# Performance work log

Hardware: AMD Instinct MI355X
Metric: run time of the kernel (lower is better)

The kernel has to match this reference:

```python
import jax, jax.numpy as jnp
import numpy as np

N = 20000      # nodes
E = 320000     # edges
DIN = 128
DOUT = 10
H = 1024
HM = 256
EPS = 1e-5


def setup_inputs() -> dict:
    key = jax.random.key(0)
    ks = jax.random.split(key, 16)
    sc = 0.02
    return {
        "x": jax.random.normal(ks[0], (N, DIN), dtype=jnp.float32),
        "edge_index": jax.random.randint(ks[1], (2, E), 0, N, dtype=jnp.int64),
        "edge_weight": jax.random.uniform(ks[2], (E,), dtype=jnp.float32),
        "W1": jax.random.normal(ks[3], (DIN, H), dtype=jnp.float32) * sc,
        "b1": jnp.zeros((H,), jnp.float32),
        "g1": jnp.ones((H,), jnp.float32),
        "beta1": jnp.zeros((H,), jnp.float32),
        "W2": jax.random.normal(ks[4], (H, H), dtype=jnp.float32) * sc,
        "b2": jnp.zeros((H,), jnp.float32),
        "g2": jnp.ones((H,), jnp.float32),
        "beta2": jnp.zeros((H,), jnp.float32),
        "Wl1": jax.random.normal(ks[5], (H, HM), dtype=jnp.float32) * sc,
        "bl1": jnp.zeros((HM,), jnp.float32),
        "Wl2": jax.random.normal(ks[6], (HM, DOUT), dtype=jnp.float32) * sc,
        "bl2": jnp.zeros((DOUT,), jnp.float32),
    }


def _gcn_conv(x, W, b, src, dst, w):
    # PyG GCNConv: linear transform, symmetric normalization (self-loops
    # already appended to src/dst/w), scatter-add aggregation at dst.
    h = x @ W                                        # [N, out]
    deg = jax.ops.segment_sum(w, dst, num_segments=N)
    dinv = jnp.where(deg > 0, jax.lax.rsqrt(deg), 0.0)
    norm = dinv[src] * w * dinv[dst]                 # [E+N]
    agg = jax.ops.segment_sum(norm[:, None] * h[src], dst, num_segments=N)
    return agg + b


def _batchnorm(x, g, b):
    m = x.mean(axis=0)
    v = jnp.mean(jnp.square(x - m), axis=0)          # biased var (torch BN)
    return g * (x - m) * jax.lax.rsqrt(v + EPS) + b


def reference(x, edge_index, edge_weight,
              W1, b1, g1, beta1, W2, b2, g2, beta2,
              Wl1, bl1, Wl2, bl2):
    loop = jnp.arange(N, dtype=edge_index.dtype)
    src = jnp.concatenate([edge_index[0], loop])
    dst = jnp.concatenate([edge_index[1], loop])
    w = jnp.concatenate([edge_weight, jnp.ones((N,), edge_weight.dtype)])

    h = jax.nn.relu(_batchnorm(_gcn_conv(x, W1, b1, src, dst, w), g1, beta1))
    h = jax.nn.relu(_batchnorm(_gcn_conv(h, W2, b2, src, dst, w), g2, beta2))
    h = jax.nn.relu(h @ Wl1 + bl1) @ Wl2 + bl2
    return jax.nn.log_softmax(h, axis=1)
```

## Files before the change

kernel.cpp:

```cpp
#include <hip/hip_runtime.h>
#include <math.h>

static constexpr int Nn  = 20000;
static constexpr int Ne  = 320000;
static constexpr int DIN = 128;
static constexpr int DOUTc = 10;
static constexpr int Hc  = 1024;
static constexpr int HMc = 256;
static constexpr float EPSc = 1e-5f;
static constexpr int NB_SCAN = (Nn + 255) / 256;

typedef __bf16 bf16_t;
typedef __bf16 bf16x8 __attribute__((ext_vector_type(8)));
typedef __bf16 bf16x4 __attribute__((ext_vector_type(4)));
typedef float  f32x4  __attribute__((ext_vector_type(4)));

__device__ __forceinline__ void gload_lds16(const bf16_t* g, bf16_t* lds) {
    __builtin_amdgcn_global_load_lds(
        (const __attribute__((address_space(1))) void*)g,
        (__attribute__((address_space(3))) void*)lds, 16, 0, 0);
}

__global__ __launch_bounds__(256) void deg_init_k(float* __restrict__ deg, int* __restrict__ cnt) {
    int i = blockIdx.x * 256 + threadIdx.x;
    if (i < Nn) { deg[i] = 1.0f; cnt[i] = 0; }
}

__global__ __launch_bounds__(256)
void deg_edge_k(const float* __restrict__ w, const int* __restrict__ dstv,
                float* __restrict__ deg, int* __restrict__ cnt) {
    int e = blockIdx.x * 256 + threadIdx.x;
    if (e < Ne) {
        int d = dstv[e];
        atomicAdd(&deg[d], w[e]);
        atomicAdd(&cnt[d], 1);
    }
}

__global__ __launch_bounds__(256) void dinv_k(float* __restrict__ deg) {
    int i = blockIdx.x * 256 + threadIdx.x;
    if (i < Nn) deg[i] = rsqrtf(deg[i]);
}

__global__ __launch_bounds__(256)
void scanA_k(const int* __restrict__ cnt, int* __restrict__ row_ptr, int* __restrict__ blk)
{
    __shared__ int wsum[4];
    int b = blockIdx.x, tid = threadIdx.x, lane = tid & 63, wv = tid >> 6;
    int i = b * 256 + tid;
    int v = (i < Nn) ? cnt[i] : 0;
    int s = v;
    #pragma unroll
    for (int off = 1; off < 64; off <<= 1) {
        int t = __shfl_up(s, off, 64);
        if (lane >= off) s += t;
    }
    if (lane == 63) wsum[wv] = s;
    __syncthreads();
    int wo = 0;
    #pragma unroll
    for (int k = 0; k < 4; ++k) if (k < wv) wo += wsum[k];
    if (i < Nn) row_ptr[i] = wo + s - v;
    if (tid == 255) blk[b] = wo + s;
}

__global__ __launch_bounds__(128)
void scanB_k(int* __restrict__ blk)
{
    __shared__ int w0;
    int tid = threadIdx.x, lane = tid & 63, wv = tid >> 6;
    int v = (tid < NB_SCAN) ? blk[tid] : 0;
    int s = v;
    #pragma unroll
    for (int off = 1; off < 64; off <<= 1) {
        int t = __shfl_up(s, off, 64);
        if (lane >= off) s += t;
    }
    if (tid == 63) w0 = s;
    __syncthreads();
    int excl = s - v + (wv ? w0 : 0);
    if (tid < NB_SCAN) blk[tid] = excl;
}

__global__ __launch_bounds__(256)
void scanC_k(int* __restrict__ row_ptr, const int* __restrict__ blk, int* __restrict__ cursor)
{
    int b = blockIdx.x;
    int i = b * 256 + threadIdx.x;
    if (i < Nn) {
        int r = row_ptr[i] + blk[b];
        row_ptr[i] = r;
        cursor[i]  = r;
    }
    if (i == 0) row_ptr[Nn] = Ne;
}

__global__ __launch_bounds__(256)
void csr_fill_k(const int* __restrict__ srcv, const int* __restrict__ dstv,
                const float* __restrict__ w, const float* __restrict__ dinv,
                int* __restrict__ cursor, int* __restrict__ csr_src,
                float* __restrict__ csr_coeff)
{
    int e = blockIdx.x * 256 + threadIdx.x;
    if (e >= Ne) return;
    int s = srcv[e], d = dstv[e];
    int pos = atomicAdd(&cursor[d], 1);
    csr_src[pos]   = s;
    csr_coeff[pos] = dinv[s] * w[e] * dinv[d];
}

__global__ __launch_bounds__(256)
void spmm_x_k(const bf16x8* __restrict__ x8, const int* __restrict__ row_ptr,
              const int* __restrict__ csr_src, const float* __restrict__ csr_coeff,
              const float* __restrict__ dinv, bf16x8* __restrict__ out8)
{
    int panel = blockIdx.x & 3;
    int node  = (blockIdx.x >> 2) * 64 + (threadIdx.x >> 2);
    if (node >= Nn) return;
    int f = (threadIdx.x & 3) + panel * 4;
    float c = dinv[node]; c = c * c;
    bf16x8 hv = x8[(size_t)node * 16 + f];
    float acc[8];
    #pragma unroll
    for (int i = 0; i < 8; ++i) acc[i] = c * (float)hv[i];
    int beg = row_ptr[node], end = row_ptr[node + 1];
    for (int j = beg; j < end; ++j) {
        int   s  = csr_src[j];
        float cf = csr_coeff[j];
        bf16x8 v = x8[(size_t)s * 16 + f];
        #pragma unroll
        for (int i = 0; i < 8; ++i) acc[i] = fmaf(cf, (float)v[i], acc[i]);
    }
    bf16x8 o;
    #pragma unroll
    for (int i = 0; i < 8; ++i) o[i] = (bf16_t)acc[i];
    out8[(size_t)node * 16 + f] = o;
}

__global__ __launch_bounds__(256)
void spmm_h_k(const bf16x8* __restrict__ h8, const int* __restrict__ row_ptr,
              const int* __restrict__ csr_src, const float* __restrict__ csr_coeff,
              const float* __restrict__ dinv, bf16x8* __restrict__ out8)
{
    int panel = blockIdx.x & 7;
    int node  = (blockIdx.x >> 3) * 16 + (threadIdx.x >> 4);
    int f     = (threadIdx.x & 15) + panel * 16;
    float c = dinv[node]; c = c * c;
    bf16x8 hv = h8[(size_t)node * 128 + f];
    float acc[8];
    #pragma unroll
    for (int i = 0; i < 8; ++i) acc[i] = c * (float)hv[i];
    int beg = row_ptr[node], end = row_ptr[node + 1];
    for (int j = beg; j < end; ++j) {
        int   s  = csr_src[j];
        float cf = csr_coeff[j];
        bf16x8 v = h8[(size_t)s * 128 + f];
        #pragma unroll
        for (int i = 0; i < 8; ++i) acc[i] = fmaf(cf, (float)v[i], acc[i]);
    }
    bf16x8 o;
    #pragma unroll
    for (int i = 0; i < 8; ++i) o[i] = (bf16_t)acc[i];
    out8[(size_t)node * 128 + f] = o;
}

template<int RK, int CN>
__global__ __launch_bounds__(256)
void transpose_bf16_k(const float* __restrict__ W, bf16_t* __restrict__ Wt)
{
    __shared__ float tile[32][33];
    int bx = blockIdx.x * 32;
    int by = blockIdx.y * 32;
    int tx = threadIdx.x & 31, ty = threadIdx.x >> 5;
    #pragma unroll
    for (int p = 0; p < 32; p += 8)
        tile[ty + p][tx] = W[(size_t)(by + ty + p) * CN + bx + tx];
    __syncthreads();
    #pragma unroll
    for (int p = 0; p < 32; p += 8)
        Wt[(size_t)(bx + ty + p) * RK + by + tx] = (bf16_t)tile[tx][ty + p];
}

__global__ __launch_bounds__(256)
void cvt_bf16_k(const float4* __restrict__ in, bf16x4* __restrict__ out, int n4)
{
    int i = blockIdx.x * 256 + threadIdx.x;
    if (i >= n4) return;
    float4 v = in[i];
    bf16x4 o = { (bf16_t)v.x, (bf16_t)v.y, (bf16_t)v.z, (bf16_t)v.w };
    out[i] = o;
}

template<int NC, int KD, bool BIAS, bool RELU, bool OUTBF, bool STATS>
__global__ __launch_bounds__(256)
void gemm_bf16_k(const bf16_t* __restrict__ A, const bf16_t* __restrict__ Bt,
                 const float* __restrict__ bias, void* __restrict__ Cv, int M,
                 float* __restrict__ s1g, float* __restrict__ s2g)
{
    __shared__ __align__(16) bf16_t Asm[128 * 32];
    __shared__ __align__(16) bf16_t Bsm[128 * 32];
    const int tid  = threadIdx.x;
    const int w    = tid >> 6;
    const int lane = tid & 63;
    const int bm = blockIdx.y * 128, bn = blockIdx.x * 128;
    const int l15 = lane & 15, quad = lane >> 4;
    const int wm = (w & 1) * 64, wn = (w >> 1) * 64;
    const int swz = quad ^ ((l15 >> 1) & 3);

    const int srow = lane >> 2;
    const int scol = 8 * ((lane & 3) ^ ((lane >> 3) & 3));
    const int c0 = w * 32;
    int ga0 = bm + c0 + srow;       if (ga0 >= M) ga0 = M - 1;
    int ga1 = bm + c0 + 16 + srow;  if (ga1 >= M) ga1 = M - 1;
    const bf16_t* gA0 = A + (size_t)ga0 * KD + scol;
    const bf16_t* gA1 = A + (size_t)ga1 * KD + scol;
    const bf16_t* gB0 = Bt + (size_t)(bn + c0 + srow) * KD + scol;
    const bf16_t* gB1 = gB0 + (size_t)16 * KD;
    bf16_t* lA0 = Asm + (c0 +  0) * 32;
    bf16_t* lA1 = Asm + (c0 + 16) * 32;
    bf16_t* lB0 = Bsm + (c0 +  0) * 32;
    bf16_t* lB1 = Bsm + (c0 + 16) * 32;

    const bf16_t* pA = Asm + (wm + l15) * 32 + swz * 8;
    const bf16_t* pB = Bsm + (wn + l15) * 32 + swz * 8;

    f32x4 acc[4][4] = {};

    for (int k0 = 0; k0 < KD; k0 += 32) {
        gload_lds16(gA0 + k0, lA0);
        gload_lds16(gA1 + k0, lA1);
        gload_lds16(gB0 + k0, lB0);
        gload_lds16(gB1 + k0, lB1);
        __syncthreads();
        bf16x8 af[4], bfr[4];
        #pragma unroll
        for (int t = 0; t < 4; ++t) {
            af[t]  = *(const bf16x8*)(pA + t * 16 * 32);
            bfr[t] = *(const bf16x8*)(pB + t * 16 * 32);
        }
        #pragma unroll
        for (int mt = 0; mt < 4; ++mt)
            #pragma unroll
            for (int nt = 0; nt < 4; ++nt)
                acc[mt][nt] = __builtin_amdgcn_mfma_f32_16x16x32_bf16(
                    af[mt], bfr[nt], acc[mt][nt], 0, 0, 0);
        __syncthreads();
    }

    #pragma unroll
    for (int mt = 0; mt < 4; ++mt) {
        #pragma unroll
        for (int r = 0; r < 4; ++r) {
            int row = bm + wm + mt * 16 + quad * 4 + r;
            if (row >= M) continue;
            #pragma unroll
            for (int nt = 0; nt < 4; ++nt) {
                int col = bn + wn + nt * 16 + l15;
                float v = acc[mt][nt][r];
                if (BIAS) v += bias[col];
                if (RELU) v = fmaxf(v, 0.f);
                if (OUTBF) ((bf16_t*)Cv)[(size_t)row * NC + col] = (bf16_t)v;
                else       ((float*)Cv)[(size_t)row * NC + col] = v;
            }
        }
    }

    if (STATS) {
        #pragma unroll
        for (int nt = 0; nt < 4; ++nt) {
            float ps = 0.f, pq = 0.f;
            #pragma unroll
            for (int mt = 0; mt < 4; ++mt)
                #pragma unroll
                for (int r = 0; r < 4; ++r) {
                    int row = bm + wm + mt * 16 + quad * 4 + r;
                    if (row < M) {
                        float v = acc[mt][nt][r];
                        ps += v;
                        pq = fmaf(v, v, pq);
                    }
                }
            ps += __shfl_down(ps, 32, 64); ps += __shfl_down(ps, 16, 64);
            pq += __shfl_down(pq, 32, 64); pq += __shfl_down(pq, 16, 64);
            if (quad == 0) {
                int col = bn + wn + nt * 16 + l15;
                atomicAdd(&s1g[col], ps);
                atomicAdd(&s2g[col], pq);
            }
        }
    }
}

__global__ __launch_bounds__(256) void zero_stats_k(float* __restrict__ s) {
    int i = blockIdx.x * 256 + threadIdx.x;
    s[i] = 0.f;
}

__global__ __launch_bounds__(256)
void bn_stats_k(const bf16_t* __restrict__ x, float* __restrict__ s1, float* __restrict__ s2)
{
    int c = blockIdx.x * 256 + threadIdx.x;
    int r0 = blockIdx.y * 250;
    float s = 0.f, q = 0.f;
    const bf16_t* p = x + (size_t)r0 * Hc + c;
    for (int r = 0; r < 250; ++r) {
        float v = (float)p[(size_t)r * Hc];
        s += v;
        q = fmaf(v, v, q);
    }
    atomicAdd(&s1[c], s);
    atomicAdd(&s2[c], q);
}

__global__ __launch_bounds__(256)
void bn_apply_k(const bf16x8* __restrict__ x8, const float* __restrict__ s1,
                const float* __restrict__ s2, const float* __restrict__ g,
                const float* __restrict__ beta, bf16x8* __restrict__ out8)
{
    int idx = blockIdx.x * 256 + threadIdx.x;
    int c8 = (idx & 127) << 3;
    bf16x8 v = x8[idx];
    bf16x8 o;
    #pragma unroll
    for (int i = 0; i < 8; ++i) {
        int c = c8 + i;
        float mean = s1[c] * (1.0f / Nn);
        float var  = s2[c] * (1.0f / Nn) - mean * mean;
        float sc = g[c] * rsqrtf(var + EPSc);
        float sh = beta[c] - mean * sc;
        o[i] = (bf16_t)fmaxf(fmaf((float)v[i], sc, sh), 0.f);
    }
    out8[idx] = o;
}

__global__ __launch_bounds__(256)
void head_k(const float* __restrict__ z, const float* __restrict__ Wl2,
            const float* __restrict__ bl2, float* __restrict__ out)
{
    int wave = threadIdx.x >> 6;
    int lane = threadIdx.x & 63;
    int node = blockIdx.x * 4 + wave;
    const float4 zv = *(const float4*)(z + (size_t)node * HMc + lane * 4);
    float p[DOUTc];
    #pragma unroll
    for (int j = 0; j < DOUTc; ++j) p[j] = 0.f;
    const float zz[4] = {zv.x, zv.y, zv.z, zv.w};
    #pragma unroll
    for (int i = 0; i < 4; ++i) {
        int k = lane * 4 + i;
        const float* wrow = Wl2 + (size_t)k * DOUTc;
        #pragma unroll
        for (int j = 0; j < DOUTc; ++j) p[j] = fmaf(zz[i], wrow[j], p[j]);
    }
    #pragma unroll
    for (int j = 0; j < DOUTc; ++j) {
        #pragma unroll
        for (int off = 32; off > 0; off >>= 1) p[j] += __shfl_down(p[j], off, 64);
    }
    if (lane == 0) {
        float v[DOUTc];
        float m = -1e30f;
        #pragma unroll
        for (int j = 0; j < DOUTc; ++j) { v[j] = p[j] + bl2[j]; m = fmaxf(m, v[j]); }
        float s = 0.f;
        #pragma unroll
        for (int j = 0; j < DOUTc; ++j) s += expf(v[j] - m);
        float ls = logf(s) + m;
        #pragma unroll
        for (int j = 0; j < DOUTc; ++j) out[(size_t)node * DOUTc + j] = v[j] - ls;
    }
}

extern "C" void kernel_launch(void* const* d_in, const int* in_sizes, int n_in,
                              void* d_out, int out_size, void* d_ws, size_t ws_size,
                              hipStream_t stream)
{
    (void)in_sizes; (void)n_in; (void)out_size; (void)ws_size;
    const float* x    = (const float*)d_in[0];
    const int*   ei   = (const int*)d_in[1];
    const float* ew   = (const float*)d_in[2];
    const float* W1   = (const float*)d_in[3];
    const float* gam1 = (const float*)d_in[5];
    const float* bet1 = (const float*)d_in[6];
    const float* W2   = (const float*)d_in[7];
    const float* gam2 = (const float*)d_in[9];
    const float* bet2 = (const float*)d_in[10];
    const float* Wl1  = (const float*)d_in[11];
    const float* bl1  = (const float*)d_in[12];
    const float* Wl2  = (const float*)d_in[13];
    const float* bl2  = (const float*)d_in[14];
    float* out = (float*)d_out;

    float* zhead = (float*)d_ws;
    float* dinv  = zhead + (size_t)Nn * HMc;
    float* s1    = dinv + Nn;
    float* s2    = s1 + Hc;
    int*   cnt      = (int*)(s2 + Hc);
    int*   row_ptr  = cnt + Nn;
    int*   cursor   = row_ptr + Nn + 16;
    int*   blk      = cursor + Nn;
    int*   csr_src  = blk + 128;
    float* csr_coef = (float*)(csr_src + Ne);
    bf16_t* xb   = (bf16_t*)(csr_coef + Ne);
    bf16_t* xagg = xb + (size_t)Nn * DIN;
    bf16_t* hgem = xagg + (size_t)Nn * DIN;
    bf16_t* hbf  = hgem + (size_t)Nn * Hc;
    bf16_t* W1t  = hbf + (size_t)Nn * Hc;
    bf16_t* W2t  = W1t + (size_t)Hc * DIN;
    bf16_t* Wl1t = W2t + (size_t)Hc * Hc;

    const int* srcv = ei;
    const int* dstv = ei + Ne;

    deg_init_k<<<(Nn + 255) / 256, 256, 0, stream>>>(dinv, cnt);
    deg_edge_k<<<(Ne + 255) / 256, 256, 0, stream>>>(ew, dstv, dinv, cnt);
    dinv_k<<<(Nn + 255) / 256, 256, 0, stream>>>(dinv);
    scanA_k<<<NB_SCAN, 256, 0, stream>>>(cnt, row_ptr, blk);
    scanB_k<<<1, 128, 0, stream>>>(blk);
    scanC_k<<<NB_SCAN, 256, 0, stream>>>(row_ptr, blk, cursor);
    csr_fill_k<<<(Ne + 255) / 256, 256, 0, stream>>>(srcv, dstv, ew, dinv, cursor,
                                                     csr_src, csr_coef);
    transpose_bf16_k<DIN, Hc><<<dim3(Hc / 32, DIN / 32), 256, 0, stream>>>(W1, W1t);
    transpose_bf16_k<Hc, Hc><<<dim3(Hc / 32, Hc / 32), 256, 0, stream>>>(W2, W2t);
    transpose_bf16_k<Hc, HMc><<<dim3(HMc / 32, Hc / 32), 256, 0, stream>>>(Wl1, Wl1t);
    cvt_bf16_k<<<(Nn * DIN / 4 + 255) / 256, 256, 0, stream>>>(
        (const float4*)x, (bf16x4*)xb, Nn * DIN / 4);

    const int MB = (Nn + 127) / 128;

    spmm_x_k<<<4 * ((Nn + 63) / 64), 256, 0, stream>>>(
        (const bf16x8*)xb, row_ptr, csr_src, csr_coef, dinv, (bf16x8*)xagg);
    zero_stats_k<<<8, 256, 0, stream>>>(s1);
    gemm_bf16_k<Hc, DIN, false, false, true, true><<<dim3(Hc / 128, MB), 256, 0, stream>>>(
        xagg, W1t, nullptr, hgem, Nn, s1, s2);
    bn_apply_k<<<Nn * Hc / 8 / 256, 256, 0, stream>>>(
        (const bf16x8*)hgem, s1, s2, gam1, bet1, (bf16x8*)hbf);

    gemm_bf16_k<Hc, Hc, false, false, true, false><<<dim3(Hc / 128, MB), 256, 0, stream>>>(
        hbf, W2t, nullptr, hgem, Nn, nullptr, nullptr);
    spmm_h_k<<<8 * (Nn / 16), 256, 0, stream>>>(
        (const bf16x8*)hgem, row_ptr, csr_src, csr_coef, dinv, (bf16x8*)hbf);
    zero_stats_k<<<8, 256, 0, stream>>>(s1);
    bn_stats_k<<<dim3(Hc / 256, 80), 256, 0, stream>>>(hbf, s1, s2);
    bn_apply_k<<<Nn * Hc / 8 / 256, 256, 0, stream>>>(
        (const bf16x8*)hbf, s1, s2, gam2, bet2, (bf16x8*)hgem);

    gemm_bf16_k<HMc, Hc, true, true, false, false><<<dim3(HMc / 128, MB), 256, 0, stream>>>(
        hgem, Wl1t, bl1, zhead, Nn, nullptr, nullptr);
    head_k<<<Nn / 4, 256, 0, stream>>>(zhead, Wl2, bl2, out);
}
```

Before: 461.9 us.

## Split layer-2 SpMM into two column-half passes and fold small setup kernels

After: 644.2 us. 39.5% more time.

```diff
diff --git a/kernel.cpp b/kernel.cpp
--- a/kernel.cpp
+++ b/kernel.cpp
@@ -21,9 +21,12 @@
         (__attribute__((address_space(3))) void*)lds, 16, 0, 0);
 }
 
-__global__ __launch_bounds__(256) void deg_init_k(float* __restrict__ deg, int* __restrict__ cnt) {
+__global__ __launch_bounds__(256)
+void deg_init_k(float* __restrict__ deg, int* __restrict__ cnt, float* __restrict__ stats)
+{
     int i = blockIdx.x * 256 + threadIdx.x;
     if (i < Nn) { deg[i] = 1.0f; cnt[i] = 0; }
+    if (i < 4 * Hc) stats[i] = 0.f;
 }
 
 __global__ __launch_bounds__(256)
@@ -37,17 +40,14 @@
     }
 }
 
-__global__ __launch_bounds__(256) void dinv_k(float* __restrict__ deg) {
-    int i = blockIdx.x * 256 + threadIdx.x;
-    if (i < Nn) deg[i] = rsqrtf(deg[i]);
-}
-
-__global__ __launch_bounds__(256)
-void scanA_k(const int* __restrict__ cnt, int* __restrict__ row_ptr, int* __restrict__ blk)
+__global__ __launch_bounds__(256)
+void scanA_k(const int* __restrict__ cnt, int* __restrict__ row_ptr, int* __restrict__ blk,
+             float* __restrict__ deg)
 {
     __shared__ int wsum[4];
     int b = blockIdx.x, tid = threadIdx.x, lane = tid & 63, wv = tid >> 6;
     int i = b * 256 + tid;
+    if (i < Nn) deg[i] = rsqrtf(deg[i]);
     int v = (i < Nn) ? cnt[i] : 0;
     int s = v;
     #pragma unroll
@@ -125,8 +125,8 @@
     for (int i = 0; i < 8; ++i) acc[i] = c * (float)hv[i];
     int beg = row_ptr[node], end = row_ptr[node + 1];
     for (int j = beg; j < end; ++j) {
-        int   s  = csr_src[j];
-        float cf = csr_coeff[j];
+        int   s  = __builtin_nontemporal_load(csr_src + j);
+        float cf = __builtin_nontemporal_load(csr_coeff + j);
         bf16x8 v = x8[(size_t)s * 16 + f];
         #pragma unroll
         for (int i = 0; i < 8; ++i) acc[i] = fmaf(cf, (float)v[i], acc[i]);
@@ -140,11 +140,11 @@
 __global__ __launch_bounds__(256)
 void spmm_h_k(const bf16x8* __restrict__ h8, const int* __restrict__ row_ptr,
               const int* __restrict__ csr_src, const float* __restrict__ csr_coeff,
-              const float* __restrict__ dinv, bf16x8* __restrict__ out8)
-{
-    int panel = blockIdx.x & 7;
-    int node  = (blockIdx.x >> 3) * 16 + (threadIdx.x >> 4);
-    int f     = (threadIdx.x & 15) + panel * 16;
+              const float* __restrict__ dinv, bf16x8* __restrict__ out8, int pass)
+{
+    int hp   = (blockIdx.x & 7) + pass * 8;
+    int node = (blockIdx.x >> 3) * 32 + (threadIdx.x >> 3);
+    int f    = (threadIdx.x & 7) + hp * 8;
     float c = dinv[node]; c = c * c;
     bf16x8 hv = h8[(size_t)node * 128 + f];
     float acc[8];
@@ -152,8 +152,8 @@
     for (int i = 0; i < 8; ++i) acc[i] = c * (float)hv[i];
     int beg = row_ptr[node], end = row_ptr[node + 1];
     for (int j = beg; j < end; ++j) {
-        int   s  = csr_src[j];
-        float cf = csr_coeff[j];
+        int   s  = __builtin_nontemporal_load(csr_src + j);
+        float cf = __builtin_nontemporal_load(csr_coeff + j);
         bf16x8 v = h8[(size_t)s * 128 + f];
         #pragma unroll
         for (int i = 0; i < 8; ++i) acc[i] = fmaf(cf, (float)v[i], acc[i]);
@@ -291,11 +291,6 @@
     }
 }
 
-__global__ __launch_bounds__(256) void zero_stats_k(float* __restrict__ s) {
-    int i = blockIdx.x * 256 + threadIdx.x;
-    s[i] = 0.f;
-}
-
 __global__ __launch_bounds__(256)
 void bn_stats_k(const bf16_t* __restrict__ x, float* __restrict__ s1, float* __restrict__ s2)
 {
@@ -393,9 +388,9 @@
 
     float* zhead = (float*)d_ws;
     float* dinv  = zhead + (size_t)Nn * HMc;
-    float* s1    = dinv + Nn;
-    float* s2    = s1 + Hc;
-    int*   cnt      = (int*)(s2 + Hc);
+    float* stats = dinv + Nn;
+    float* s1a = stats, *s2a = stats + Hc, *s1b = stats + 2 * Hc, *s2b = stats + 3 * Hc;
+    int*   cnt      = (int*)(stats + 4 * Hc);
     int*   row_ptr  = cnt + Nn;
     int*   cursor   = row_ptr + Nn + 16;
     int*   blk      = cursor + Nn;
@@ -412,10 +407,9 @@
     const int* srcv = ei;
     const int* dstv = ei + Ne;
 
-    deg_init_k<<<(Nn + 255) / 256, 256, 0, stream>>>(dinv, cnt);
+    deg_init_k<<<NB_SCAN, 256, 0, stream>>>(dinv, cnt, stats);
     deg_edge_k<<<(Ne + 255) / 256, 256, 0, stream>>>(ew, dstv, dinv, cnt);
-    dinv_k<<<(Nn + 255) / 256, 256, 0, stream>>>(dinv);
-    scanA_k<<<NB_SCAN, 256, 0, stream>>>(cnt, row_ptr, blk);
+    scanA_k<<<NB_SCAN, 256, 0, stream>>>(cnt, row_ptr, blk, dinv);
     scanB_k<<<1, 128, 0, stream>>>(blk);
     scanC_k<<<NB_SCAN, 256, 0, stream>>>(row_ptr, blk, cursor);
     csr_fill_k<<<(Ne + 255) / 256, 256, 0, stream>>>(srcv, dstv, ew, dinv, cursor,
@@ -430,20 +424,20 @@
 
     spmm_x_k<<<4 * ((Nn + 63) / 64), 256, 0, stream>>>(
         (const bf16x8*)xb, row_ptr, csr_src, csr_coef, dinv, (bf16x8*)xagg);
-    zero_stats_k<<<8, 256, 0, stream>>>(s1);
     gemm_bf16_k<Hc, DIN, false, false, true, true><<<dim3(Hc / 128, MB), 256, 0, stream>>>(
-        xagg, W1t, nullptr, hgem, Nn, s1, s2);
+        xagg, W1t, nullptr, hgem, Nn, s1a, s2a);
     bn_apply_k<<<Nn * Hc / 8 / 256, 256, 0, stream>>>(
-        (const bf16x8*)hgem, s1, s2, gam1, bet1, (bf16x8*)hbf);
+        (const bf16x8*)hgem, s1a, s2a, gam1, bet1, (bf16x8*)hbf);
 
     gemm_bf16_k<Hc, Hc, false, false, true, false><<<dim3(Hc / 128, MB), 256, 0, stream>>>(
         hbf, W2t, nullptr, hgem, Nn, nullptr, nullptr);
-    spmm_h_k<<<8 * (Nn / 16), 256, 0, stream>>>(
-        (const bf16x8*)hgem, row_ptr, csr_src, csr_coef, dinv, (bf16x8*)hbf);
-    zero_stats_k<<<8, 256, 0, stream>>>(s1);
-    bn_stats_k<<<dim3(Hc / 256, 80), 256, 0, stream>>>(hbf, s1, s2);
+    spmm_h_k<<<8 * (Nn / 32), 256, 0, stream>>>(
+        (const bf16x8*)hgem, row_ptr, csr_src, csr_coef, dinv, (bf16x8*)hbf, 0);
+    spmm_h_k<<<8 * (Nn / 32), 256, 0, stream>>>(
+        (const bf16x8*)hgem, row_ptr, csr_src, csr_coef, dinv, (bf16x8*)hbf, 1);
+    bn_stats_k<<<dim3(Hc / 256, 80), 256, 0, stream>>>(hbf, s1b, s2b);
     bn_apply_k<<<Nn * Hc / 8 / 256, 256, 0, stream>>>(
-        (const bf16x8*)hbf, s1, s2, gam2, bet2, (bf16x8*)hgem);
+        (const bf16x8*)hbf, s1b, s2b, gam2, bet2, (bf16x8*)hgem);
 
     gemm_bf16_k<HMc, Hc, true, true, false, false><<<dim3(HMc / 128, MB), 256, 0, stream>>>(
         hgem, Wl1t, bl1, zhead, Nn, nullptr, nullptr);
```
